# Kernel optimization log

Measured on AMD Instinct MI355X. Metric: run time of the kernel, lower is better.

Reference implementation:

```python
import jax, jax.numpy as jnp
import numpy as np

B, S, D, H = 2, 2048, 1024, 16
HD = D // H

def setup_inputs() -> dict:
    key = jax.random.key(0)
    ks = jax.random.split(key, 5)
    x = jax.random.normal(ks[0], (B, S, D), dtype=jnp.float32)
    scale = float(np.sqrt(6.0 / (D + D)))  # xavier_uniform bound
    def xavier(k):
        return jax.random.uniform(k, (D, D), dtype=jnp.float32, minval=-scale, maxval=scale)
    WQ, WK, WV, WO = xavier(ks[1]), xavier(ks[2]), xavier(ks[3]), xavier(ks[4])
    # causal mask, 1 = valid, 0 = masked, shape (B, 1, S_q, S_k)
    mask = jnp.broadcast_to(jnp.tril(jnp.ones((S, S), dtype=jnp.int32)), (B, 1, S, S))
    return {"x": x, "WQ": WQ, "WK": WK, "WV": WV, "WO": WO, "mask": mask}

def reference(x, WQ, WK, WV, WO, mask):
    b, s, d = x.shape
    # projections and head split: (B, H, S, HD)
    def split_heads(t):
        return t.reshape(b, s, H, HD).transpose(0, 2, 1, 3)
    q = split_heads(x @ WQ)
    k = split_heads(x @ WK)
    v = split_heads(x @ WV)
    scores = jnp.einsum('bhqd,bhkd->bhqk', q, k) / jnp.sqrt(jnp.float32(HD))
    neg = jnp.finfo(scores.dtype).min
    scores = jnp.where(mask == 0, neg, scores)
    attn = jax.nn.softmax(scores, axis=-1)
    out = jnp.einsum('bhqk,bhkd->bhqd', attn, v)  # (B, H, S, HD)
    out = out.transpose(0, 2, 1, 3).reshape(b, s, d)
    return out @ WO
```

## Files before the change

kernel.cpp:

```cpp
#include <hip/hip_runtime.h>
#include <hip/hip_bf16.h>


typedef __attribute__((ext_vector_type(8))) short short8;
typedef __attribute__((ext_vector_type(4))) float floatx4;
typedef __attribute__((ext_vector_type(4))) unsigned short ushort4v;
typedef __attribute__((ext_vector_type(2))) unsigned int uint2v;

#define GLDS16(gp, lp) __builtin_amdgcn_global_load_lds( \
    (const __attribute__((address_space(1))) void*)(gp), \
    (__attribute__((address_space(3))) void*)(lp), 16, 0, 0)

#define EXP2F(x) __builtin_amdgcn_exp2f(x)
#define NEG_INF (-__builtin_inff())

__device__ __forceinline__ unsigned short f2bf(float f) {
  unsigned int u = __builtin_bit_cast(unsigned int, f);
  return (unsigned short)((u + 0x7fffu + ((u >> 16) & 1u)) >> 16);
}
__device__ __forceinline__ float bf2f(unsigned short h) {
  unsigned int u = ((unsigned int)h) << 16;
  return __builtin_bit_cast(float, u);
}
__device__ __forceinline__ unsigned int pack2bf(float a, float b) {
#if __has_builtin(__builtin_amdgcn_cvt_pk_bf16_f32)
  auto r = __builtin_amdgcn_cvt_pk_bf16_f32(a, b);
  return __builtin_bit_cast(unsigned int, r);
#else
  unsigned int ua = (__builtin_bit_cast(unsigned int, a) + 0x8000u) >> 16;
  unsigned int ub = (__builtin_bit_cast(unsigned int, b) + 0x8000u) & 0xFFFF0000u;
  return ua | ub;
#endif
}
__device__ __forceinline__ floatx4 mfma16(short8 a, short8 b, floatx4 c) {
  return __builtin_amdgcn_mfma_f32_16x16x32_bf16(a, b, c, 0, 0, 0);
}

__global__ void k_convert_x(const float* __restrict__ x, unsigned short* __restrict__ xb) {
  int i = (blockIdx.x * 256 + threadIdx.x) * 4;
  ushort4v o;
  o.x = f2bf(x[i + 0]);
  o.y = f2bf(x[i + 1]);
  o.z = f2bf(x[i + 2]);
  o.w = f2bf(x[i + 3]);
  *(ushort4v*)(xb + i) = o;
}

__global__ void k_transpose_w(const float* __restrict__ WQ, const float* __restrict__ WK,
                              const float* __restrict__ WV, const float* __restrict__ WO,
                              unsigned short* __restrict__ wtq, unsigned short* __restrict__ wto) {
  __shared__ float tile[32][33];
  const float* W = (blockIdx.z == 0) ? WQ : (blockIdx.z == 1) ? WK : (blockIdx.z == 2) ? WV : WO;
  unsigned short* dst = (blockIdx.z < 3) ? (wtq + (size_t)blockIdx.z * 1024 * 1024) : wto;
  int tx = threadIdx.x & 31, ty = threadIdx.x >> 5;
  int bx = blockIdx.x, by = blockIdx.y;
#pragma unroll
  for (int j = 0; j < 4; ++j)
    tile[ty + j * 8][tx] = W[(size_t)(by * 32 + ty + j * 8) * 1024 + bx * 32 + tx];
  __syncthreads();
#pragma unroll
  for (int j = 0; j < 4; ++j)
    dst[(size_t)(bx * 32 + ty + j * 8) * 1024 + by * 32 + tx] = f2bf(tile[tx][ty + j * 8]);
}

template <int MODE>
__global__ __launch_bounds__(256, 2) void k_gemm(
    const unsigned short* __restrict__ A, const unsigned short* __restrict__ BT,
    float* __restrict__ Cf, unsigned short* __restrict__ Qp,
    unsigned short* __restrict__ Kp, unsigned short* __restrict__ Vt, int K) {
  __shared__ __align__(16) unsigned short smem[128 * 136];
  unsigned short* lA = smem;
  unsigned short* lB = smem + 128 * 64;
  const int tid = threadIdx.x;
  const int wave = tid >> 6, lane = tid & 63;
  const int wm = wave & 1, wn = wave >> 1;
  const int m0 = blockIdx.x * 128, n0 = blockIdx.y * 128;
  const int l15 = lane & 15, l16 = lane >> 4;
  const int r8 = lane >> 3, c8 = lane & 7;
  const int gchunk = (c8 ^ r8) << 3;

  floatx4 acc[4][4] = {};
  for (int k0 = 0; k0 < K; k0 += 64) {
    __syncthreads();
#pragma unroll
    for (int i = 0; i < 4; ++i) {
      int seg = wave * 4 + i;
      int row = seg * 8 + r8;
      GLDS16(A + (size_t)(m0 + row) * K + k0 + gchunk, lA + seg * 512);
      GLDS16(BT + (size_t)(n0 + row) * K + k0 + gchunk, lB + seg * 512);
    }
    __syncthreads();
#pragma unroll
    for (int ks = 0; ks < 2; ++ks) {
      short8 af[4], bfr[4];
#pragma unroll
      for (int t = 0; t < 4; ++t) {
        int m = wm * 64 + t * 16 + l15;
        int cl = ks * 4 + l16;
        af[t] = *(const short8*)(lA + m * 64 + ((cl ^ (m & 7)) << 3));
        int n = wn * 64 + t * 16 + l15;
        bfr[t] = *(const short8*)(lB + n * 64 + ((cl ^ (n & 7)) << 3));
      }
#pragma unroll
      for (int mt = 0; mt < 4; ++mt)
#pragma unroll
        for (int nt = 0; nt < 4; ++nt)
          acc[mt][nt] = mfma16(af[mt], bfr[nt], acc[mt][nt]);
    }
  }
  const int sel = n0 >> 10;
  if (MODE == 1) {
#pragma unroll
    for (int mt = 0; mt < 4; ++mt)
#pragma unroll
      for (int nt = 0; nt < 4; ++nt)
#pragma unroll
        for (int r = 0; r < 4; ++r) {
          int m = m0 + wm * 64 + mt * 16 + l16 * 4 + r;
          int n = n0 + wn * 64 + nt * 16 + l15;
          Cf[(size_t)m * 1024 + n] = acc[mt][nt][r];
        }
  } else if (sel < 2) {
    unsigned short* dst = (sel == 0) ? Qp : Kp;
    __syncthreads();
#pragma unroll
    for (int mt = 0; mt < 4; ++mt)
#pragma unroll
      for (int nt = 0; nt < 4; ++nt)
#pragma unroll
        for (int r = 0; r < 4; ++r) {
          int ml = wm * 64 + mt * 16 + l16 * 4 + r;
          int nl = wn * 64 + nt * 16 + l15;
          smem[ml * 136 + nl] = f2bf(acc[mt][nt][r]);
        }
    __syncthreads();
    const int b = m0 >> 11, s0 = m0 & 2047;
    const int h0 = (n0 & 1023) >> 6;
#pragma unroll
    for (int it = 0; it < 8; ++it) {
      int ml = it * 16 + (tid >> 4);
      int c = (tid & 15) * 8;
      short8 v = *(const short8*)(smem + ml * 136 + c);
      int h = h0 + (c >> 6), hd = c & 63;
      *(short8*)(dst + ((size_t)((b * 16 + h) * 2048 + s0 + ml) << 6) + hd) = v;
    }
  } else {
    __syncthreads();
#pragma unroll
    for (int mt = 0; mt < 4; ++mt)
#pragma unroll
      for (int nt = 0; nt < 4; ++nt)
#pragma unroll
        for (int r = 0; r < 4; ++r) {
          int nl = wn * 64 + nt * 16 + l15;
          int ml = wm * 64 + mt * 16 + l16 * 4 + r;
          smem[nl * 136 + ml] = f2bf(acc[mt][nt][r]);
        }
    __syncthreads();
    const int b = m0 >> 11, s0 = m0 & 2047;
    const int h0 = (n0 - 2048) >> 6;
#pragma unroll
    for (int it = 0; it < 8; ++it) {
      int nl = it * 16 + (tid >> 4);
      int sc = (tid & 15) * 8;
      short8 v = *(const short8*)(smem + nl * 136 + sc);
      int hh = h0 + (nl >> 6), hd = nl & 63;
      *(short8*)(Vt + ((size_t)(b * 16 + hh) * 64 + hd) * 2048 + s0 + sc) = v;
    }
  }
}

__global__ __launch_bounds__(256, 2) void k_attn(
    const unsigned short* __restrict__ Qp, const unsigned short* __restrict__ Kp,
    const unsigned short* __restrict__ Vt, unsigned short* __restrict__ O) {
  __shared__ __align__(16) unsigned short kvbuf[2][2][64 * 64];
  __shared__ __align__(16) unsigned short pbuf[4][32 * 64];
  const int tid = threadIdx.x, wave = tid >> 6, lane = tid & 63;
  const int bh = blockIdx.x & 31;
  const int rest = blockIdx.x >> 5;
  const int p = rest & 7, half = rest >> 3;
  const int qt = (wave < 2) ? (15 - p) : p;
  const int wsub = (wave & 1) + 2 * half;
  const int l15 = lane & 15, l16 = lane >> 4;
  const int r8 = lane >> 3, c8 = lane & 7;
  const int gchunk = (c8 ^ r8) << 3;
  const int R0 = qt * 128 + wsub * 32;
  const size_t base = (size_t)bh << 17;
  unsigned short* pb = &pbuf[wave][0];

  const float qscale = 0.125f * 1.44269504088896f;
  short8 qf[2][2];
#pragma unroll
  for (int mt = 0; mt < 2; ++mt)
#pragma unroll
    for (int ks = 0; ks < 2; ++ks) {
      short8 v = *(const short8*)(Qp + base + (size_t)(R0 + mt * 16 + l15) * 64 + ks * 32 + l16 * 8);
#pragma unroll
      for (int j = 0; j < 8; ++j) {
        float f = bf2f((unsigned short)v[j]) * qscale;
        v[j] = (short)f2bf(f);
      }
      qf[mt][ks] = v;
    }
  short8 onesv;
#pragma unroll
  for (int j = 0; j < 8; ++j) onesv[j] = (short)0x3F80;

  floatx4 oacc[4][2] = {};
  floatx4 lacc[2] = {};

#define STAGE(KT, BUF) \
  { _Pragma("unroll") for (int i_ = 0; i_ < 2; ++i_) { \
      int seg_ = wave * 2 + i_; \
      GLDS16(Kp + base + (size_t)((KT) * 64 + seg_ * 8 + r8) * 64 + gchunk, \
             &kvbuf[BUF][0][0] + seg_ * 512); \
      GLDS16(Vt + base + (size_t)(seg_ * 8 + r8) * 2048 + (KT) * 64 + gchunk, \
             &kvbuf[BUF][1][0] + seg_ * 512); \
    } }

  STAGE(0, 0);
  for (int kt = 0; kt < 32; ++kt) {
    const int cb = kt & 1;
    __syncthreads();
    if (kt + 1 < 32) STAGE(kt + 1, cb ^ 1);
    if (kt * 64 > R0 + 31) continue;
    const unsigned short* kb = &kvbuf[cb][0][0];
    const unsigned short* vb = &kvbuf[cb][1][0];

    floatx4 sacc[2][4] = {};
#pragma unroll
    for (int ks = 0; ks < 2; ++ks) {
      short8 kfr[4];
#pragma unroll
      for (int nt = 0; nt < 4; ++nt) {
        int row = nt * 16 + l15;
        int cl = ks * 4 + l16;
        kfr[nt] = *(const short8*)(kb + row * 64 + ((cl ^ (row & 7)) << 3));
      }
#pragma unroll
      for (int mt = 0; mt < 2; ++mt)
#pragma unroll
        for (int nt = 0; nt < 4; ++nt)
          sacc[mt][nt] = mfma16(kfr[nt], qf[mt][ks], sacc[mt][nt]);
    }
    if (kt * 64 + 63 > R0) {
#pragma unroll
      for (int mt = 0; mt < 2; ++mt)
#pragma unroll
        for (int nt = 0; nt < 4; ++nt)
#pragma unroll
          for (int rr = 0; rr < 4; ++rr) {
            int key = kt * 64 + nt * 16 + l16 * 4 + rr;
            int qrow = R0 + mt * 16 + l15;
            if (key > qrow) sacc[mt][nt][rr] = NEG_INF;
          }
    }
#pragma unroll
    for (int mt = 0; mt < 2; ++mt)
#pragma unroll
      for (int nt = 0; nt < 4; ++nt) {
        uint2v pk;
        pk.x = pack2bf(EXP2F(sacc[mt][nt][0]), EXP2F(sacc[mt][nt][1]));
        pk.y = pack2bf(EXP2F(sacc[mt][nt][2]), EXP2F(sacc[mt][nt][3]));
        int q = mt * 16 + l15;
        int ch = (nt * 4 + l16) ^ ((q & 7) << 1);
        *(uint2v*)(pb + q * 64 + ch * 4) = pk;
      }
    short8 pfr[2][2];
#pragma unroll
    for (int mt = 0; mt < 2; ++mt)
#pragma unroll
      for (int ks = 0; ks < 2; ++ks) {
        int q = mt * 16 + l15;
        int ch = (ks * 8 + l16 * 2) ^ ((q & 7) << 1);
        pfr[mt][ks] = *(const short8*)(pb + q * 64 + ch * 4);
      }
#pragma unroll
    for (int ks = 0; ks < 2; ++ks) {
      short8 vf[4];
#pragma unroll
      for (int ht = 0; ht < 4; ++ht) {
        int row = ht * 16 + l15;
        int cl = ks * 4 + l16;
        vf[ht] = *(const short8*)(vb + row * 64 + ((cl ^ (row & 7)) << 3));
      }
#pragma unroll
      for (int mt = 0; mt < 2; ++mt) {
        lacc[mt] = mfma16(onesv, pfr[mt][ks], lacc[mt]);
#pragma unroll
        for (int ht = 0; ht < 4; ++ht)
          oacc[ht][mt] = mfma16(vf[ht], pfr[mt][ks], oacc[ht][mt]);
      }
    }
  }
#undef STAGE

  const int b = bh >> 4, h = bh & 15;
  float inv[2];
#pragma unroll
  for (int mt = 0; mt < 2; ++mt) inv[mt] = 1.0f / lacc[mt][0];
#pragma unroll
  for (int ht = 0; ht < 4; ++ht)
#pragma unroll
    for (int mt = 0; mt < 2; ++mt) {
      int srow = R0 + mt * 16 + l15;
      uint2v pk;
      pk.x = pack2bf(oacc[ht][mt][0] * inv[mt], oacc[ht][mt][1] * inv[mt]);
      pk.y = pack2bf(oacc[ht][mt][2] * inv[mt], oacc[ht][mt][3] * inv[mt]);
      *(uint2v*)(O + (size_t)(b * 2048 + srow) * 1024 + h * 64 + ht * 16 + l16 * 4) = pk;
    }
}

extern "C" void kernel_launch(void* const* d_in, const int* in_sizes, int n_in,
                              void* d_out, int out_size, void* d_ws, size_t ws_size,
                              hipStream_t stream) {
  const float* x = (const float*)d_in[0];
  const float* WQ = (const float*)d_in[1];
  const float* WK = (const float*)d_in[2];
  const float* WV = (const float*)d_in[3];
  const float* WO = (const float*)d_in[4];
  float* out = (float*)d_out;
  char* ws = (char*)d_ws;
  unsigned short* xb = (unsigned short*)(ws);
  unsigned short* wtq = (unsigned short*)(ws + 8388608);
  unsigned short* wto = (unsigned short*)(ws + 14680064);
  unsigned short* Qp = (unsigned short*)(ws + 16777216);
  unsigned short* Kp = (unsigned short*)(ws + 25165824);
  unsigned short* Vt = (unsigned short*)(ws + 33554432);
  unsigned short* Ob = (unsigned short*)(ws + 41943040);

  k_convert_x<<<dim3(4096), dim3(256), 0, stream>>>(x, xb);
  k_transpose_w<<<dim3(32, 32, 4), dim3(256), 0, stream>>>(WQ, WK, WV, WO, wtq, wto);
  k_gemm<0><<<dim3(32, 24), dim3(256), 0, stream>>>(xb, wtq, (float*)nullptr, Qp, Kp, Vt, 1024);
  k_attn<<<dim3(512), dim3(256), 0, stream>>>(Qp, Kp, Vt, Ob);
  k_gemm<1><<<dim3(32, 8), dim3(256), 0, stream>>>(Ob, wto, out, (unsigned short*)nullptr,
                                                   (unsigned short*)nullptr,
                                                   (unsigned short*)nullptr, 1024);
}
```

Baseline: 193.3 us.

## Split causal attention along keys with atomic job queue and combine kernel

Attention work is reorganized into 1024 jobs, each a 128-row query tile with half of its causal key range, taken largest first from a global atomic counter by persistent blocks. Partial unnormalized outputs and row sums go to fp32 scratch, and a new combine kernel adds the two halves, normalizes, and writes bf16. The goal is better load balance over the triangular workload. The cost is an extra kernel launch, fp32 partial-result traffic, and atomic scheduling overhead.

```diff
diff --git a/kernel.cpp b/kernel.cpp
--- a/kernel.cpp
+++ b/kernel.cpp
@@ -48,7 +48,9 @@
 
 __global__ void k_transpose_w(const float* __restrict__ WQ, const float* __restrict__ WK,
                               const float* __restrict__ WV, const float* __restrict__ WO,
-                              unsigned short* __restrict__ wtq, unsigned short* __restrict__ wto) {
+                              unsigned short* __restrict__ wtq, unsigned short* __restrict__ wto,
+                              int* __restrict__ counter) {
+  if (threadIdx.x == 0 && blockIdx.x == 0 && blockIdx.y == 0 && blockIdx.z == 0) *counter = 0;
   __shared__ float tile[32][33];
   const float* W = (blockIdx.z == 0) ? WQ : (blockIdx.z == 1) ? WK : (blockIdx.z == 2) ? WV : WO;
   unsigned short* dst = (blockIdx.z < 3) ? (wtq + (size_t)blockIdx.z * 1024 * 1024) : wto;
@@ -172,42 +174,20 @@
 
 __global__ __launch_bounds__(256, 2) void k_attn(
     const unsigned short* __restrict__ Qp, const unsigned short* __restrict__ Kp,
-    const unsigned short* __restrict__ Vt, unsigned short* __restrict__ O) {
+    const unsigned short* __restrict__ Vt, float* __restrict__ Opart,
+    float* __restrict__ lpart, int* __restrict__ counter) {
   __shared__ __align__(16) unsigned short kvbuf[2][2][64 * 64];
   __shared__ __align__(16) unsigned short pbuf[4][32 * 64];
+  __shared__ int sjob;
   const int tid = threadIdx.x, wave = tid >> 6, lane = tid & 63;
-  const int bh = blockIdx.x & 31;
-  const int rest = blockIdx.x >> 5;
-  const int p = rest & 7, half = rest >> 3;
-  const int qt = (wave < 2) ? (15 - p) : p;
-  const int wsub = (wave & 1) + 2 * half;
   const int l15 = lane & 15, l16 = lane >> 4;
   const int r8 = lane >> 3, c8 = lane & 7;
   const int gchunk = (c8 ^ r8) << 3;
-  const int R0 = qt * 128 + wsub * 32;
-  const size_t base = (size_t)bh << 17;
   unsigned short* pb = &pbuf[wave][0];
-
   const float qscale = 0.125f * 1.44269504088896f;
-  short8 qf[2][2];
-#pragma unroll
-  for (int mt = 0; mt < 2; ++mt)
-#pragma unroll
-    for (int ks = 0; ks < 2; ++ks) {
-      short8 v = *(const short8*)(Qp + base + (size_t)(R0 + mt * 16 + l15) * 64 + ks * 32 + l16 * 8);
-#pragma unroll
-      for (int j = 0; j < 8; ++j) {
-        float f = bf2f((unsigned short)v[j]) * qscale;
-        v[j] = (short)f2bf(f);
-      }
-      qf[mt][ks] = v;
-    }
   short8 onesv;
 #pragma unroll
   for (int j = 0; j < 8; ++j) onesv[j] = (short)0x3F80;
-
-  floatx4 oacc[4][2] = {};
-  floatx4 lacc[2] = {};
 
 #define STAGE(KT, BUF) \
   { _Pragma("unroll") for (int i_ = 0; i_ < 2; ++i_) { \
@@ -218,97 +198,168 @@
              &kvbuf[BUF][1][0] + seg_ * 512); \
     } }
 
-  STAGE(0, 0);
-  for (int kt = 0; kt < 32; ++kt) {
-    const int cb = kt & 1;
-    __syncthreads();
-    if (kt + 1 < 32) STAGE(kt + 1, cb ^ 1);
-    if (kt * 64 > R0 + 31) continue;
-    const unsigned short* kb = &kvbuf[cb][0][0];
-    const unsigned short* vb = &kvbuf[cb][1][0];
-
-    floatx4 sacc[2][4] = {};
-#pragma unroll
-    for (int ks = 0; ks < 2; ++ks) {
-      short8 kfr[4];
-#pragma unroll
-      for (int nt = 0; nt < 4; ++nt) {
-        int row = nt * 16 + l15;
-        int cl = ks * 4 + l16;
-        kfr[nt] = *(const short8*)(kb + row * 64 + ((cl ^ (row & 7)) << 3));
+  for (;;) {
+    __syncthreads();
+    if (tid == 0) sjob = atomicAdd(counter, 1);
+    __syncthreads();
+    const int job = sjob;
+    if (job >= 1024) break;
+    const int qt = 15 - (job >> 6);
+    const int half = (job >> 5) & 1;
+    const int bh = job & 31;
+    const int kt0 = half ? (qt + 1) : 0;
+    const int kt1 = half ? (2 * qt + 2) : (qt + 1);
+    const int R0 = qt * 128 + wave * 32;
+    const size_t base = (size_t)bh << 17;
+
+    short8 qf[2][2];
+#pragma unroll
+    for (int mt = 0; mt < 2; ++mt)
+#pragma unroll
+      for (int ks = 0; ks < 2; ++ks) {
+        short8 v = *(const short8*)(Qp + base + (size_t)(R0 + mt * 16 + l15) * 64 +
+                                    ks * 32 + l16 * 8);
+#pragma unroll
+        for (int j = 0; j < 8; ++j) {
+          float f = bf2f((unsigned short)v[j]) * qscale;
+          v[j] = (short)f2bf(f);
+        }
+        qf[mt][ks] = v;
+      }
+
+    floatx4 oacc[4][2] = {};
+    floatx4 lacc[2] = {};
+
+    STAGE(kt0, 0);
+    for (int kt = kt0; kt < kt1; ++kt) {
+      const int cb = (kt - kt0) & 1;
+      __syncthreads();
+      if (kt + 1 < kt1) STAGE(kt + 1, cb ^ 1);
+      if (kt * 64 > R0 + 31) continue;
+      const unsigned short* kb = &kvbuf[cb][0][0];
+      const unsigned short* vb = &kvbuf[cb][1][0];
+
+      floatx4 sacc[2][4] = {};
+#pragma unroll
+      for (int ks = 0; ks < 2; ++ks) {
+        short8 kfr[4];
+#pragma unroll
+        for (int nt = 0; nt < 4; ++nt) {
+          int row = nt * 16 + l15;
+          int cl = ks * 4 + l16;
+          kfr[nt] = *(const short8*)(kb + row * 64 + ((cl ^ (row & 7)) << 3));
+        }
+#pragma unroll
+        for (int mt = 0; mt < 2; ++mt)
+#pragma unroll
+          for (int nt = 0; nt < 4; ++nt)
+            sacc[mt][nt] = mfma16(kfr[nt], qf[mt][ks], sacc[mt][nt]);
+      }
+      if (kt * 64 + 63 > R0) {
+#pragma unroll
+        for (int mt = 0; mt < 2; ++mt)
+#pragma unroll
+          for (int nt = 0; nt < 4; ++nt)
+#pragma unroll
+            for (int rr = 0; rr < 4; ++rr) {
+              int key = kt * 64 + nt * 16 + l16 * 4 + rr;
+              int qrow = R0 + mt * 16 + l15;
+              if (key > qrow) sacc[mt][nt][rr] = NEG_INF;
+            }
       }
 #pragma unroll
       for (int mt = 0; mt < 2; ++mt)
 #pragma unroll
-        for (int nt = 0; nt < 4; ++nt)
-          sacc[mt][nt] = mfma16(kfr[nt], qf[mt][ks], sacc[mt][nt]);
-    }
-    if (kt * 64 + 63 > R0) {
+        for (int nt = 0; nt < 4; ++nt) {
+          uint2v pk;
+          pk.x = pack2bf(EXP2F(sacc[mt][nt][0]), EXP2F(sacc[mt][nt][1]));
+          pk.y = pack2bf(EXP2F(sacc[mt][nt][2]), EXP2F(sacc[mt][nt][3]));
+          int q = mt * 16 + l15;
+          int ch = (nt * 4 + l16) ^ ((q & 7) << 1);
+          *(uint2v*)(pb + q * 64 + ch * 4) = pk;
+        }
+      short8 pfr[2][2];
 #pragma unroll
       for (int mt = 0; mt < 2; ++mt)
 #pragma unroll
-        for (int nt = 0; nt < 4; ++nt)
-#pragma unroll
-          for (int rr = 0; rr < 4; ++rr) {
-            int key = kt * 64 + nt * 16 + l16 * 4 + rr;
-            int qrow = R0 + mt * 16 + l15;
-            if (key > qrow) sacc[mt][nt][rr] = NEG_INF;
-          }
-    }
-#pragma unroll
-    for (int mt = 0; mt < 2; ++mt)
-#pragma unroll
-      for (int nt = 0; nt < 4; ++nt) {
-        uint2v pk;
-        pk.x = pack2bf(EXP2F(sacc[mt][nt][0]), EXP2F(sacc[mt][nt][1]));
-        pk.y = pack2bf(EXP2F(sacc[mt][nt][2]), EXP2F(sacc[mt][nt][3]));
-        int q = mt * 16 + l15;
-        int ch = (nt * 4 + l16) ^ ((q & 7) << 1);
-        *(uint2v*)(pb + q * 64 + ch * 4) = pk;
-      }
-    short8 pfr[2][2];
-#pragma unroll
-    for (int mt = 0; mt < 2; ++mt)
+        for (int ks = 0; ks < 2; ++ks) {
+          int q = mt * 16 + l15;
+          int ch = (ks * 8 + l16 * 2) ^ ((q & 7) << 1);
+          pfr[mt][ks] = *(const short8*)(pb + q * 64 + ch * 4);
+        }
 #pragma unroll
       for (int ks = 0; ks < 2; ++ks) {
-        int q = mt * 16 + l15;
-        int ch = (ks * 8 + l16 * 2) ^ ((q & 7) << 1);
-        pfr[mt][ks] = *(const short8*)(pb + q * 64 + ch * 4);
-      }
-#pragma unroll
-    for (int ks = 0; ks < 2; ++ks) {
-      short8 vf[4];
-#pragma unroll
-      for (int ht = 0; ht < 4; ++ht) {
-        int row = ht * 16 + l15;
-        int cl = ks * 4 + l16;
-        vf[ht] = *(const short8*)(vb + row * 64 + ((cl ^ (row & 7)) << 3));
-      }
+        short8 vf[4];
+#pragma unroll
+        for (int ht = 0; ht < 4; ++ht) {
+          int row = ht * 16 + l15;
+          int cl = ks * 4 + l16;
+          vf[ht] = *(const short8*)(vb + row * 64 + ((cl ^ (row & 7)) << 3));
+        }
+#pragma unroll
+        for (int mt = 0; mt < 2; ++mt) {
+          lacc[mt] = mfma16(onesv, pfr[mt][ks], lacc[mt]);
+#pragma unroll
+          for (int ht = 0; ht < 4; ++ht)
+            oacc[ht][mt] = mfma16(vf[ht], pfr[mt][ks], oacc[ht][mt]);
+        }
+      }
+    }
+
+    float* Os = Opart + (size_t)job * 8192;
+#pragma unroll
+    for (int ht = 0; ht < 4; ++ht)
 #pragma unroll
       for (int mt = 0; mt < 2; ++mt) {
-        lacc[mt] = mfma16(onesv, pfr[mt][ks], lacc[mt]);
-#pragma unroll
-        for (int ht = 0; ht < 4; ++ht)
-          oacc[ht][mt] = mfma16(vf[ht], pfr[mt][ks], oacc[ht][mt]);
-      }
+        int ql = wave * 32 + mt * 16 + l15;
+#pragma unroll
+        for (int r = 0; r < 4; ++r) {
+          int hd = ht * 16 + l16 * 4 + r;
+          Os[(size_t)hd * 128 + ql] = oacc[ht][mt][r];
+        }
+      }
+    if (l16 == 0) {
+      lpart[job * 128 + wave * 32 + l15] = lacc[0][0];
+      lpart[job * 128 + wave * 32 + 16 + l15] = lacc[1][0];
     }
   }
 #undef STAGE
-
+}
+
+__global__ __launch_bounds__(256, 2) void k_comb(
+    const float* __restrict__ Opart, const float* __restrict__ lpart,
+    unsigned short* __restrict__ Ob) {
+  __shared__ float lds[32][129];
+  __shared__ float linv[128];
+  const int tid = threadIdx.x;
+  const int qt = 15 - (blockIdx.x >> 5);
+  const int bh = blockIdx.x & 31;
+  const int jA = ((blockIdx.x >> 5) << 6) | bh;
+  const int jB = jA + 32;
+  const float* Oa = Opart + (size_t)jA * 8192;
+  const float* Op2 = Opart + (size_t)jB * 8192;
+  if (tid < 128) linv[tid] = 1.0f / (lpart[jA * 128 + tid] + lpart[jB * 128 + tid]);
   const int b = bh >> 4, h = bh & 15;
-  float inv[2];
-#pragma unroll
-  for (int mt = 0; mt < 2; ++mt) inv[mt] = 1.0f / lacc[mt][0];
-#pragma unroll
-  for (int ht = 0; ht < 4; ++ht)
-#pragma unroll
-    for (int mt = 0; mt < 2; ++mt) {
-      int srow = R0 + mt * 16 + l15;
-      uint2v pk;
-      pk.x = pack2bf(oacc[ht][mt][0] * inv[mt], oacc[ht][mt][1] * inv[mt]);
-      pk.y = pack2bf(oacc[ht][mt][2] * inv[mt], oacc[ht][mt][3] * inv[mt]);
-      *(uint2v*)(O + (size_t)(b * 2048 + srow) * 1024 + h * 64 + ht * 16 + l16 * 4) = pk;
-    }
+  const size_t obase = ((size_t)(b * 2048 + qt * 128)) * 1024 + h * 64;
+#pragma unroll
+  for (int c = 0; c < 2; ++c) {
+    __syncthreads();
+#pragma unroll
+    for (int i = 0; i < 16; ++i) {
+      int hdl = i * 2 + (tid >> 7);
+      int rl = tid & 127;
+      size_t off = (size_t)(c * 32 + hdl) * 128 + rl;
+      lds[hdl][rl] = Oa[off] + Op2[off];
+    }
+    __syncthreads();
+#pragma unroll
+    for (int i = 0; i < 16; ++i) {
+      int rl = i * 8 + (tid >> 5);
+      int hdl = tid & 31;
+      float v = lds[hdl][rl] * linv[rl];
+      Ob[obase + (size_t)rl * 1024 + c * 32 + hdl] = f2bf(v);
+    }
+  }
 }
 
 extern "C" void kernel_launch(void* const* d_in, const int* in_sizes, int n_in,
@@ -328,11 +379,15 @@
   unsigned short* Kp = (unsigned short*)(ws + 25165824);
   unsigned short* Vt = (unsigned short*)(ws + 33554432);
   unsigned short* Ob = (unsigned short*)(ws + 41943040);
+  int* counter = (int*)(ws + 50331648);
+  float* Opart = (float*)(ws + 50335744);
+  float* lpart = (float*)(ws + 83890176);
 
   k_convert_x<<<dim3(4096), dim3(256), 0, stream>>>(x, xb);
-  k_transpose_w<<<dim3(32, 32, 4), dim3(256), 0, stream>>>(WQ, WK, WV, WO, wtq, wto);
+  k_transpose_w<<<dim3(32, 32, 4), dim3(256), 0, stream>>>(WQ, WK, WV, WO, wtq, wto, counter);
   k_gemm<0><<<dim3(32, 24), dim3(256), 0, stream>>>(xb, wtq, (float*)nullptr, Qp, Kp, Vt, 1024);
-  k_attn<<<dim3(512), dim3(256), 0, stream>>>(Qp, Kp, Vt, Ob);
+  k_attn<<<dim3(512), dim3(256), 0, stream>>>(Qp, Kp, Vt, Opart, lpart, counter);
+  k_comb<<<dim3(512), dim3(256), 0, stream>>>(Opart, lpart, Ob);
   k_gemm<1><<<dim3(32, 8), dim3(256), 0, stream>>>(Ob, wto, out, (unsigned short*)nullptr,
                                                    (unsigned short*)nullptr,
                                                    (unsigned short*)nullptr, 1024);
```

New measurement: 197.0 us. About the same (+1.9%).
